# Optimization experiments

Measured on AMD Instinct MI355X. Metric: run time of the kernel, lower is better.

The kernel has to match this reference:

```python
import jax, jax.numpy as jnp
import numpy as np
import math

B, S, D, NH, HFF, E, K, C, L, V = 8, 256, 1024, 16, 2048, 8, 2, 10, 4, 32000
HD = D // NH
EPS = 1e-5


def _pos_encoding(max_len, d_model):
    pos = jnp.arange(max_len, dtype=jnp.float32)[:, None]
    div = jnp.exp(jnp.arange(0, d_model, 2, dtype=jnp.float32) * (-math.log(10000.0) / d_model))
    pe = jnp.zeros((max_len, d_model), dtype=jnp.float32)
    pe = pe.at[:, 0::2].set(jnp.sin(pos * div))
    pe = pe.at[:, 1::2].set(jnp.cos(pos * div))
    return pe[:, None, :]  # [max_len, 1, D], matching torch buffer layout


def _layernorm(x, g, b):
    mu = jnp.mean(x, axis=-1, keepdims=True)
    var = jnp.mean((x - mu) ** 2, axis=-1, keepdims=True)
    return (x - mu) * jax.lax.rsqrt(var + EPS) * g + b


def setup_inputs() -> dict:
    key = jax.random.key(0)
    ks = jax.random.split(key, 20)
    sc = lambda *shape: 0.02
    inp = {
        "src": jax.random.randint(ks[0], (B, S), 0, V, dtype=jnp.int32),
        "emb": jax.random.normal(ks[1], (V, D), jnp.float32) * 0.02,
        "in_proj_w": jax.random.normal(ks[2], (L, 3 * D, D), jnp.float32) * 0.02,
        "in_proj_b": jnp.zeros((L, 3 * D), jnp.float32),
        "out_w": jax.random.normal(ks[3], (L, D, D), jnp.float32) * 0.02,
        "out_b": jnp.zeros((L, D), jnp.float32),
        "ln1_g": jnp.ones((L, D), jnp.float32),
        "ln1_b": jnp.zeros((L, D), jnp.float32),
        "ln2_g": jnp.ones((L, D), jnp.float32),
        "ln2_b": jnp.zeros((L, D), jnp.float32),
        "gate_w": jax.random.normal(ks[4], (L, E, D), jnp.float32) * 0.02,
        "gate_b": jnp.zeros((L, E), jnp.float32),
        "w1": jax.random.normal(ks[5], (L, E, D, HFF), jnp.float32) * 0.02,
        "b1": jnp.zeros((L, E, HFF), jnp.float32),
        "w2": jax.random.normal(ks[6], (L, E, HFF, D), jnp.float32) * 0.02,
        "b2": jnp.zeros((L, E, D), jnp.float32),
        "cls_w": jax.random.normal(ks[7], (C, D), jnp.float32) * 0.02,
        "cls_b": jnp.zeros((C,), jnp.float32),
    }
    return inp


def _attention(x, ipw, ipb, ow, ob):
    # x: [B,S,D]
    qkv = x @ ipw.T + ipb  # [B,S,3D]
    q, k, v = jnp.split(qkv, 3, axis=-1)
    q = q.reshape(B, S, NH, HD)
    k = k.reshape(B, S, NH, HD)
    v = v.reshape(B, S, NH, HD)
    scores = jnp.einsum("bqhd,bkhd->bhqk", q, k) / math.sqrt(HD)
    attn = jax.nn.softmax(scores, axis=-1)
    o = jnp.einsum("bhqk,bkhd->bqhd", attn, v).reshape(B, S, D)
    return o @ ow.T + ob


def _moe(x, gw, gb, w1, b1, w2, b2):
    # x: [B,S,D]; gw: [E,D]; w1: [E,D,H]; w2: [E,H,D]
    t = x.reshape(B * S, D)
    logits = t @ gw.T + gb  # [T,E]
    topv, topi = jax.lax.top_k(logits, K)  # [T,K]
    weights = jax.nn.softmax(topv, axis=-1)  # [T,K]
    # dense expert compute (small E, compute-bound), combine via top-k gather
    h = jax.nn.relu(jnp.einsum("td,edh->teh", t, w1) + b1)  # [T,E,H]
    y = jnp.einsum("teh,ehd->ted", h, w2) + b2  # [T,E,D]
    sel = jnp.take_along_axis(y, topi[:, :, None], axis=1)  # [T,K,D]
    out = jnp.sum(sel * weights[:, :, None], axis=1)  # [T,D]
    return out.reshape(B, S, D), logits.reshape(B, S, E)


def reference(src, emb, in_proj_w, in_proj_b, out_w, out_b, ln1_g, ln1_b,
              ln2_g, ln2_b, gate_w, gate_b, w1, b1, w2, b2, cls_w, cls_b):
    x = emb[src] * math.sqrt(D)  # [B,S,D]
    pe = _pos_encoding(5000, D)  # [max_len,1,D]
    # faithful to original: pe indexed by batch dim (x.size(0)), broadcast over seq
    x = x + pe[:B]  # [B,1,D] -> broadcast [B,S,D]
    all_gates = []
    for l in range(in_proj_w.shape[0]):
        a = _attention(x, in_proj_w[l], in_proj_b[l], out_w[l], out_b[l])
        x = _layernorm(x + a, ln1_g[l], ln1_b[l])
        m, g = _moe(x, gate_w[l], gate_b[l], w1[l], b1[l], w2[l], b2[l])
        x = _layernorm(x + m, ln2_g[l], ln2_b[l])
        all_gates.append(g)
    pooled = jnp.mean(x, axis=1)  # [B,D]
    out = pooled @ cls_w.T + cls_b  # [B,C]
    return out, jnp.stack(all_gates)  # ([B,C], [L,B,S,E])
```

## Files before the change

kernel.cpp:

```cpp
#include <hip/hip_runtime.h>
#include <math.h>

#define TKN 2048
#define DIM 1024
#define NHEAD 16
#define HDIM 64
#define HFF 2048
#define NE 8
#define TOPK 2
#define NCLS 10
#define NLAYER 4
#define SEQ 256
#define BATCH 8

typedef __attribute__((ext_vector_type(8))) _Float16 f16x8;
typedef __attribute__((ext_vector_type(4))) float f32x4;
typedef __attribute__((ext_vector_type(8))) unsigned short u16x8;

__device__ __forceinline__ unsigned short f2h(float v) {
  _Float16 h = (_Float16)v;
  return __builtin_bit_cast(unsigned short, h);
}
__device__ __forceinline__ float h2f(unsigned short u) {
  return (float)__builtin_bit_cast(_Float16, u);
}
__device__ __forceinline__ void fsplit(float v, unsigned short& hi, unsigned short& lo) {
  _Float16 h = (_Float16)v;
  hi = __builtin_bit_cast(unsigned short, h);
  lo = f2h(v - (float)h);
}

__device__ __forceinline__ void gload_lds16(const void* g, void* l) {
  __builtin_amdgcn_global_load_lds((__attribute__((address_space(1))) void*)g,
                                   (__attribute__((address_space(3))) void*)l,
                                   16, 0, 0);
}

__global__ __launch_bounds__(256) void k_embed(const int* __restrict__ src,
                                               const float* __restrict__ emb,
                                               float* __restrict__ x,
                                               unsigned short* __restrict__ xhi,
                                               unsigned short* __restrict__ xlo) {
  const int t = blockIdx.x;
  const int tid = threadIdx.x;
  const int b = t / SEQ;
  const int tok = src[t];
  const float* erow = emb + (size_t)tok * DIM;
  const size_t base = (size_t)t * DIM;
  const float cexp = -9.210340371976184f / 1024.0f;
#pragma unroll
  for (int j = 0; j < 4; ++j) {
    int d = tid + 256 * j;
    int i2 = d & ~1;
    float ang = (float)b * expf((float)i2 * cexp);
    float pe = (d & 1) ? cosf(ang) : sinf(ang);
    float v = erow[d] * 32.0f + pe;
    x[base + d] = v;
    fsplit(v, xhi[base + d], xlo[base + d]);
  }
}

template <bool LO>
__global__ __launch_bounds__(256) void k_cvt_split(const float* __restrict__ in,
                                                   unsigned short* __restrict__ ohi,
                                                   unsigned short* __restrict__ olo) {
  int i = blockIdx.x * 256 + threadIdx.x;
  float4 v = ((const float4*)in)[i];
  ushort4 h, l;
  fsplit(v.x, h.x, l.x); fsplit(v.y, h.y, l.y);
  fsplit(v.z, h.z, l.z); fsplit(v.w, h.w, l.w);
  ((ushort4*)ohi)[i] = h;
  if (LO) ((ushort4*)olo)[i] = l;
}

template <bool LO>
__global__ __launch_bounds__(256) void k_cvt_t2(const float* __restrict__ in,
                                                unsigned short* __restrict__ ohi,
                                                unsigned short* __restrict__ olo,
                                                int R, int Cc) {
  __shared__ float ts[64][33];
  const int t = threadIdx.x;
  const int c0 = blockIdx.x * 32, r0 = blockIdx.y * 64;
  const float* ip = in + (size_t)blockIdx.z * R * Cc;
  const size_t obase = (size_t)blockIdx.z * R * Cc;
  const int cc = t & 31, rr0 = t >> 5;
#pragma unroll
  for (int j = 0; j < 8; ++j)
    ts[rr0 + 8 * j][cc] = ip[(size_t)(r0 + rr0 + 8 * j) * Cc + c0 + cc];
  __syncthreads();
  const int c = t >> 3, rch = (t & 7) * 8;
  u16x8 hv, lv;
#pragma unroll
  for (int i = 0; i < 8; ++i) {
    unsigned short hi, lo;
    fsplit(ts[rch + i][c], hi, lo);
    hv[i] = hi; lv[i] = lo;
  }
  size_t o = obase + (size_t)(c0 + c) * R + r0 + rch;
  *(u16x8*)(ohi + o) = hv;
  if (LO) *(u16x8*)(olo + o) = lv;
}

template <int MODE, bool RELU, int OUTK, bool SPLIT>
__global__ __launch_bounds__(256) void k_mfma_gemm(
    const unsigned short* __restrict__ Ahi, const unsigned short* __restrict__ Alo,
    const unsigned short* __restrict__ Bhi, const unsigned short* __restrict__ Blo,
    const float* __restrict__ bias, void* __restrict__ out0, void* __restrict__ out1,
    int M, int N, int K,
    const int* __restrict__ slot_token, const int* __restrict__ offg) {
  constexpr int NP = SPLIT ? 2 : 1;
  __shared__ unsigned short U[2][NP][128 * 64];
  const int tid = threadIdx.x;
  const int w = tid >> 6, lane = tid & 63;
  const int bm = blockIdx.y * 128, bn = blockIdx.x * 128;
  int r0 = 0, rows = M, e = 0;
  if (MODE != 0) {
    e = blockIdx.z;
    r0 = offg[e];
    rows = offg[e + 1] - r0;
    if (bm >= rows) return;
  }
  const size_t bwb = (size_t)e * K * N;
  const float* biasq = bias + (size_t)e * N;

  const int lrow8 = lane >> 3;
  const int s = (lane & 7) ^ lrow8;
  const int chunk = (s & 3) * 8;
  const unsigned short* sp0[4];
  const unsigned short* sp1[4];
#pragma unroll
  for (int i = 0; i < 4; ++i) {
    int rloc = w * 32 + i * 8 + lrow8;
    int growA;
    if (MODE == 0) {
      growA = bm + rloc;
    } else {
      int rr = bm + rloc;
      if (rr >= rows) rr = rows - 1;
      growA = (MODE == 1) ? slot_token[r0 + rr] : (r0 + rr);
    }
    size_t aoff = (size_t)growA * K + chunk;
    size_t boff = bwb + (size_t)(bn + rloc) * K + chunk;
    if constexpr (SPLIT) {
      sp0[i] = (s < 4 ? Ahi : Alo) + aoff;
      sp1[i] = (s < 4 ? Bhi : Blo) + boff;
    } else {
      sp0[i] = (s < 4) ? (Ahi + aoff) : (Bhi + boff);
      sp1[i] = nullptr;
    }
  }

  f32x4 acc[4][4] = {};
  const int wr = w >> 1, wc = w & 1;
  const int lr = lane & 15, lg = lane >> 4;
  const int sw = lr & 7;
  unsigned aoffs[4], boffs[4];
#pragma unroll
  for (int m = 0; m < 4; ++m)
    aoffs[m] = (unsigned)((wr * 64 + m * 16 + lr) * 64 + ((lg ^ sw) * 8));
#pragma unroll
  for (int n = 0; n < 4; ++n)
    boffs[n] = (unsigned)((wc * 64 + n * 16 + lr) * 64 + ((lg ^ sw) * 8));

#pragma unroll
  for (int i = 0; i < 4; ++i) {
    gload_lds16(sp0[i], &U[0][0][(w * 32 + i * 8) * 64]);
    sp0[i] += 32;
    if constexpr (SPLIT) {
      gload_lds16(sp1[i], &U[0][1][(w * 32 + i * 8) * 64]);
      sp1[i] += 32;
    }
  }
  asm volatile("s_waitcnt vmcnt(0)" ::: "memory");
  __builtin_amdgcn_s_barrier();

  const int NT = K / 32;
#pragma unroll 2
  for (int t = 0; t < NT; ++t) {
    const int cur = t & 1;
    if (t + 1 < NT) {
#pragma unroll
      for (int i = 0; i < 4; ++i) {
        gload_lds16(sp0[i], &U[cur ^ 1][0][(w * 32 + i * 8) * 64]);
        sp0[i] += 32;
        if constexpr (SPLIT) {
          gload_lds16(sp1[i], &U[cur ^ 1][1][(w * 32 + i * 8) * 64]);
          sp1[i] += 32;
        }
      }
    }
    f16x8 afh[4], bfh[4], afl[4], bfl[4];
    if constexpr (SPLIT) {
#pragma unroll
      for (int m = 0; m < 4; ++m) afh[m] = *(const f16x8*)&U[cur][0][aoffs[m]];
#pragma unroll
      for (int m = 0; m < 4; ++m) afl[m] = *(const f16x8*)&U[cur][0][aoffs[m] ^ 32];
#pragma unroll
      for (int n = 0; n < 4; ++n) bfh[n] = *(const f16x8*)&U[cur][1][boffs[n]];
#pragma unroll
      for (int n = 0; n < 4; ++n) bfl[n] = *(const f16x8*)&U[cur][1][boffs[n] ^ 32];
    } else {
#pragma unroll
      for (int m = 0; m < 4; ++m) afh[m] = *(const f16x8*)&U[cur][0][aoffs[m]];
#pragma unroll
      for (int n = 0; n < 4; ++n) bfh[n] = *(const f16x8*)&U[cur][0][boffs[n] ^ 32];
    }
#pragma unroll
    for (int m = 0; m < 4; ++m)
#pragma unroll
      for (int n = 0; n < 4; ++n) {
        acc[m][n] = __builtin_amdgcn_mfma_f32_16x16x32_f16(afh[m], bfh[n], acc[m][n], 0, 0, 0);
        if constexpr (SPLIT) {
          acc[m][n] = __builtin_amdgcn_mfma_f32_16x16x32_f16(afh[m], bfl[n], acc[m][n], 0, 0, 0);
          acc[m][n] = __builtin_amdgcn_mfma_f32_16x16x32_f16(afl[m], bfh[n], acc[m][n], 0, 0, 0);
        }
      }
    asm volatile("s_waitcnt vmcnt(0)" ::: "memory");
    __builtin_amdgcn_s_barrier();
  }

  float bv[4];
#pragma unroll
  for (int n = 0; n < 4; ++n) bv[n] = biasq[bn + wc * 64 + n * 16 + lr];

#pragma unroll
  for (int m = 0; m < 4; ++m) {
#pragma unroll
    for (int j = 0; j < 4; ++j) {
      int rowg = bm + wr * 64 + m * 16 + lg * 4 + j;
      if (MODE != 0 && rowg >= rows) continue;
      size_t crow = (size_t)((MODE == 0) ? rowg : (r0 + rowg)) * N;
#pragma unroll
      for (int n = 0; n < 4; ++n) {
        float v = acc[m][n][j] + bv[n];
        if (RELU) v = fmaxf(v, 0.f);
        size_t o = crow + bn + wc * 64 + n * 16 + lr;
        if (OUTK == 0) {
          ((float*)out0)[o] = v;
        } else if (OUTK == 1) {
          ((unsigned short*)out0)[o] = f2h(v);
        } else {
          unsigned short hi, lo;
          fsplit(v, hi, lo);
          ((unsigned short*)out0)[o] = hi;
          ((unsigned short*)out1)[o] = lo;
        }
      }
    }
  }
}

__global__ __launch_bounds__(256) void k_attn(const float* __restrict__ qkv,
                                              unsigned short* __restrict__ ohi,
                                              unsigned short* __restrict__ olo) {
  const int qt = blockIdx.x;
  const int hh = blockIdx.y;
  const int bb = blockIdx.z;
  const int tid = threadIdx.x;
  __shared__ float qs[16][64];
  __shared__ float ps[16][256];
  const int t0 = bb * SEQ + qt * 16;
  for (int i = tid; i < 16 * 64; i += 256) {
    int qi = i >> 6, d = i & 63;
    qs[qi][d] = qkv[(size_t)(t0 + qi) * (3 * DIM) + hh * 64 + d];
  }
  __syncthreads();
  float s[16];
#pragma unroll
  for (int qi = 0; qi < 16; ++qi) s[qi] = 0.f;
  const float* krow = qkv + (size_t)(bb * SEQ + tid) * (3 * DIM) + DIM + hh * 64;
#pragma unroll 4
  for (int c = 0; c < 16; ++c) {
    float4 kv = *(const float4*)(krow + c * 4);
#pragma unroll
    for (int qi = 0; qi < 16; ++qi) {
      s[qi] += kv.x * qs[qi][c * 4 + 0] + kv.y * qs[qi][c * 4 + 1] +
               kv.z * qs[qi][c * 4 + 2] + kv.w * qs[qi][c * 4 + 3];
    }
  }
#pragma unroll
  for (int qi = 0; qi < 16; ++qi) ps[qi][tid] = s[qi] * 0.125f;
  __syncthreads();
  const int wv = tid >> 6, lane = tid & 63;
  for (int rr = wv; rr < 16; rr += 4) {
    float v[4];
#pragma unroll
    for (int j = 0; j < 4; ++j) v[j] = ps[rr][lane + 64 * j];
    float m = fmaxf(fmaxf(v[0], v[1]), fmaxf(v[2], v[3]));
    for (int msk = 32; msk; msk >>= 1) m = fmaxf(m, __shfl_xor(m, msk));
    float e[4], sum = 0.f;
#pragma unroll
    for (int j = 0; j < 4; ++j) { e[j] = expf(v[j] - m); sum += e[j]; }
    for (int msk = 32; msk; msk >>= 1) sum += __shfl_xor(sum, msk);
    float inv = 1.0f / sum;
#pragma unroll
    for (int j = 0; j < 4; ++j) ps[rr][lane + 64 * j] = e[j] * inv;
  }
  __syncthreads();
  const int qi0 = tid >> 6, d = tid & 63;
  float acc[4] = {0.f, 0.f, 0.f, 0.f};
  const float* vbase = qkv + (size_t)(bb * SEQ) * (3 * DIM) + 2 * DIM + hh * 64 + d;
  for (int k = 0; k < 256; ++k) {
    float vv = vbase[(size_t)k * (3 * DIM)];
    acc[0] += ps[qi0][k] * vv;
    acc[1] += ps[qi0 + 4][k] * vv;
    acc[2] += ps[qi0 + 8][k] * vv;
    acc[3] += ps[qi0 + 12][k] * vv;
  }
#pragma unroll
  for (int j = 0; j < 4; ++j) {
    size_t o = (size_t)(t0 + qi0 + 4 * j) * DIM + hh * 64 + d;
    fsplit(acc[j], ohi[o], olo[o]);
  }
}

__device__ __forceinline__ float block_reduce_sum(float v, float* red) {
  const int tid = threadIdx.x;
  red[tid] = v;
  __syncthreads();
  for (int s = 128; s > 0; s >>= 1) {
    if (tid < s) red[tid] += red[tid + s];
    __syncthreads();
  }
  float r = red[0];
  __syncthreads();
  return r;
}

__global__ __launch_bounds__(256) void k_add_ln(const float* __restrict__ xin,
                                                const float* __restrict__ add,
                                                const float* __restrict__ g,
                                                const float* __restrict__ bt,
                                                float* __restrict__ xout,
                                                unsigned short* __restrict__ xhi,
                                                unsigned short* __restrict__ xlo) {
  __shared__ float red[256];
  const int t = blockIdx.x, tid = threadIdx.x;
  const size_t base = (size_t)t * DIM;
  float v[4];
  float s = 0.f;
#pragma unroll
  for (int j = 0; j < 4; ++j) {
    int d = tid + 256 * j;
    v[j] = xin[base + d] + add[base + d];
    s += v[j];
  }
  float mean = block_reduce_sum(s, red) * (1.0f / DIM);
  float s2 = 0.f;
#pragma unroll
  for (int j = 0; j < 4; ++j) { float dv = v[j] - mean; s2 += dv * dv; }
  float var = block_reduce_sum(s2, red) * (1.0f / DIM);
  float rs = rsqrtf(var + 1e-5f);
#pragma unroll
  for (int j = 0; j < 4; ++j) {
    int d = tid + 256 * j;
    float o = (v[j] - mean) * rs * g[d] + bt[d];
    xout[base + d] = o;
    fsplit(o, xhi[base + d], xlo[base + d]);
  }
}

__global__ __launch_bounds__(256) void k_gate(const float* __restrict__ x,
                                              const float* __restrict__ gw,
                                              const float* __restrict__ gb,
                                              float* __restrict__ gout,
                                              int* __restrict__ topi,
                                              float* __restrict__ topw) {
  __shared__ float xs[DIM];
  __shared__ float lgs[NE];
  const int t = blockIdx.x, tid = threadIdx.x;
#pragma unroll
  for (int j = 0; j < 4; ++j) xs[tid + 256 * j] = x[(size_t)t * DIM + tid + 256 * j];
  __syncthreads();
  const int eg = tid >> 5, l32 = tid & 31;
  const float* wrow = gw + (size_t)eg * DIM;
  float p = 0.f;
  for (int j = 0; j < 32; ++j) {
    int d = l32 + 32 * j;
    p += xs[d] * wrow[d];
  }
  for (int m = 16; m; m >>= 1) p += __shfl_xor(p, m);
  if (l32 == 0) lgs[eg] = p;
  __syncthreads();
  if (tid < NE) {
    float v = lgs[tid] + gb[tid];
    gout[(size_t)t * NE + tid] = v;
    lgs[tid] = v;
  }
  __syncthreads();
  if (tid == 0) {
    int i0 = 0; float v0 = lgs[0];
    for (int i = 1; i < NE; ++i) if (lgs[i] > v0) { v0 = lgs[i]; i0 = i; }
    int i1 = -1; float v1 = -1e30f;
    for (int i = 0; i < NE; ++i) { if (i == i0) continue; if (lgs[i] > v1) { v1 = lgs[i]; i1 = i; } }
    float e1 = expf(v1 - v0);
    float w0 = 1.0f / (1.0f + e1);
    topi[2 * t] = i0; topi[2 * t + 1] = i1;
    topw[2 * t] = w0; topw[2 * t + 1] = e1 * w0;
  }
}

__global__ __launch_bounds__(512) void k_route(const int* __restrict__ topi,
                                               int* __restrict__ offg,
                                               int* __restrict__ slot_token,
                                               int* __restrict__ slot_of) {
  __shared__ int cnt_s[NE];
  __shared__ int off_s[NE + 1];
  const int tid = threadIdx.x;
  const int w = tid >> 6, lane = tid & 63;
  int c = 0;
  for (int i = lane; i < TKN * TOPK; i += 64) c += (topi[i] == w) ? 1 : 0;
  for (int m = 32; m; m >>= 1) c += __shfl_xor(c, m);
  if (lane == 0) cnt_s[w] = c;
  __syncthreads();
  if (tid == 0) {
    off_s[0] = 0;
    for (int e2 = 0; e2 < NE; ++e2) off_s[e2 + 1] = off_s[e2] + cnt_s[e2];
    for (int e2 = 0; e2 <= NE; ++e2) offg[e2] = off_s[e2];
  }
  __syncthreads();
  int base = off_s[w];
  for (int i0 = 0; i0 < TKN * TOPK; i0 += 64) {
    int i = i0 + lane;
    bool mm = (topi[i] == w);
    unsigned long long mask = __ballot(mm ? 1 : 0);
    int rank = __popcll(mask & ((1ull << lane) - 1ull));
    if (mm) {
      int slot = base + rank;
      slot_token[slot] = i >> 1;
      slot_of[i] = slot;
    }
    base += __popcll(mask);
  }
}

__global__ __launch_bounds__(256) void k_moe_combine_ln(const float* __restrict__ xin,
                                                        const float* __restrict__ y,
                                                        const float* __restrict__ topw,
                                                        const int* __restrict__ slot_of,
                                                        const float* __restrict__ g,
                                                        const float* __restrict__ bt,
                                                        float* __restrict__ xout,
                                                        unsigned short* __restrict__ xhi,
                                                        unsigned short* __restrict__ xlo) {
  __shared__ float red[256];
  const int t = blockIdx.x, tid = threadIdx.x;
  const float w0 = topw[2 * t], w1v = topw[2 * t + 1];
  const int s0 = slot_of[2 * t], s1 = slot_of[2 * t + 1];
  const size_t base = (size_t)t * DIM;
  float v[4];
  float s = 0.f;
#pragma unroll
  for (int j = 0; j < 4; ++j) {
    int d = tid + 256 * j;
    v[j] = xin[base + d] + w0 * y[(size_t)s0 * DIM + d] + w1v * y[(size_t)s1 * DIM + d];
    s += v[j];
  }
  float mean = block_reduce_sum(s, red) * (1.0f / DIM);
  float s2 = 0.f;
#pragma unroll
  for (int j = 0; j < 4; ++j) { float dv = v[j] - mean; s2 += dv * dv; }
  float var = block_reduce_sum(s2, red) * (1.0f / DIM);
  float rs = rsqrtf(var + 1e-5f);
#pragma unroll
  for (int j = 0; j < 4; ++j) {
    int d = tid + 256 * j;
    float o = (v[j] - mean) * rs * g[d] + bt[d];
    xout[base + d] = o;
    fsplit(o, xhi[base + d], xlo[base + d]);
  }
}

__global__ __launch_bounds__(256) void k_pool_cls(const float* __restrict__ x,
                                                  const float* __restrict__ cw,
                                                  const float* __restrict__ cb,
                                                  float* __restrict__ out) {
  __shared__ float pooled[DIM];
  const int b = blockIdx.x, tid = threadIdx.x;
  float a[4] = {0.f, 0.f, 0.f, 0.f};
  for (int s = 0; s < SEQ; ++s) {
    const float* row = x + (size_t)(b * SEQ + s) * DIM;
#pragma unroll
    for (int j = 0; j < 4; ++j) a[j] += row[tid + 256 * j];
  }
#pragma unroll
  for (int j = 0; j < 4; ++j) pooled[tid + 256 * j] = a[j] * (1.0f / SEQ);
  __syncthreads();
  const int wv = tid >> 6, lane = tid & 63;
  for (int c = wv; c < NCLS; c += 4) {
    float p = 0.f;
    for (int d = lane; d < DIM; d += 64) p += pooled[d] * cw[(size_t)c * DIM + d];
    for (int m = 32; m; m >>= 1) p += __shfl_xor(p, m);
    if (lane == 0) out[b * NCLS + c] = p + cb[c];
  }
}

extern "C" void kernel_launch(void* const* d_in, const int* in_sizes, int n_in,
                              void* d_out, int out_size, void* d_ws, size_t ws_size,
                              hipStream_t stream) {
  const int*   src  = (const int*)  d_in[0];
  const float* emb  = (const float*)d_in[1];
  const float* ipw  = (const float*)d_in[2];
  const float* ipb  = (const float*)d_in[3];
  const float* ow   = (const float*)d_in[4];
  const float* ob   = (const float*)d_in[5];
  const float* ln1g = (const float*)d_in[6];
  const float* ln1b = (const float*)d_in[7];
  const float* ln2g = (const float*)d_in[8];
  const float* ln2b = (const float*)d_in[9];
  const float* gw   = (const float*)d_in[10];
  const float* gb   = (const float*)d_in[11];
  const float* w1   = (const float*)d_in[12];
  const float* b1   = (const float*)d_in[13];
  const float* w2   = (const float*)d_in[14];
  const float* b2   = (const float*)d_in[15];
  const float* cw   = (const float*)d_in[16];
  const float* cb   = (const float*)d_in[17];
  float* out = (float*)d_out;

  char* ws = (char*)d_ws;
  size_t off = 0;
  auto carve = [&](size_t bytes) -> void* {
    void* p = ws + off;
    off += (bytes + 255) & ~(size_t)255;
    return p;
  };
  float*          x     = (float*)carve((size_t)TKN * DIM * 4);
  unsigned short* xhi   = (unsigned short*)carve((size_t)TKN * DIM * 2);
  unsigned short* xlo   = (unsigned short*)carve((size_t)TKN * DIM * 2);
  char*           bufQ  = (char*)carve((size_t)2 * TKN * TOPK * HFF * 2);
  float*          qkv   = (float*)bufQ;
  unsigned short* h_hi  = (unsigned short*)bufQ;
  unsigned short* h_lo  = (unsigned short*)(bufQ + (size_t)TKN * TOPK * HFF * 2);
  unsigned short* at_hi = (unsigned short*)carve((size_t)TKN * DIM * 2);
  unsigned short* at_lo = (unsigned short*)carve((size_t)TKN * DIM * 2);
  char*           bufP  = (char*)carve((size_t)TKN * TOPK * DIM * 4);
  float*          proj  = (float*)bufP;
  float*          ybuf  = (float*)bufP;
  unsigned short* wq_hi = (unsigned short*)carve((size_t)3 * DIM * DIM * 2);
  unsigned short* wq_lo = (unsigned short*)carve((size_t)3 * DIM * DIM * 2);
  unsigned short* wo_hi = (unsigned short*)carve((size_t)DIM * DIM * 2);
  unsigned short* wo_lo = (unsigned short*)carve((size_t)DIM * DIM * 2);
  unsigned short* wt_hi = (unsigned short*)carve((size_t)NE * DIM * HFF * 2);
  unsigned short* wt_lo = (unsigned short*)carve((size_t)NE * DIM * HFF * 2);
  float* topw       = (float*)carve((size_t)TKN * TOPK * 4);
  int*   topi       = (int*)  carve((size_t)TKN * TOPK * 4);
  int*   slot_token = (int*)  carve((size_t)TKN * TOPK * 4);
  int*   slot_of    = (int*)  carve((size_t)TKN * TOPK * 4);
  int*   offg       = (int*)  carve(64);

  k_embed<<<TKN, 256, 0, stream>>>(src, emb, x, xhi, xlo);

  for (int l = 0; l < NLAYER; ++l) {
    const float* ipw_l = ipw + (size_t)l * 3 * DIM * DIM;
    const float* ow_l  = ow  + (size_t)l * DIM * DIM;
    const float* w1_l  = w1  + (size_t)l * NE * DIM * HFF;
    const float* w2_l  = w2  + (size_t)l * NE * HFF * DIM;
    const bool spd = (l < 3);
    const bool spm = (l < 2);

    if (spd) {
      k_cvt_split<true><<<(3 * DIM * DIM) / 1024, 256, 0, stream>>>(ipw_l, wq_hi, wq_lo);
      k_cvt_split<true><<<(DIM * DIM) / 1024, 256, 0, stream>>>(ow_l, wo_hi, wo_lo);
    } else {
      k_cvt_split<false><<<(3 * DIM * DIM) / 1024, 256, 0, stream>>>(ipw_l, wq_hi, wq_lo);
      k_cvt_split<false><<<(DIM * DIM) / 1024, 256, 0, stream>>>(ow_l, wo_hi, wo_lo);
    }
    if (spm)
      k_cvt_t2<true><<<dim3(HFF / 32, DIM / 64, NE), 256, 0, stream>>>(w1_l, wt_hi, wt_lo, DIM, HFF);
    else
      k_cvt_t2<false><<<dim3(HFF / 32, DIM / 64, NE), 256, 0, stream>>>(w1_l, wt_hi, wt_lo, DIM, HFF);

    if (spd)
      k_mfma_gemm<0, false, 0, true><<<dim3(3 * DIM / 128, TKN / 128), 256, 0, stream>>>(
          xhi, xlo, wq_hi, wq_lo, ipb + (size_t)l * 3 * DIM, qkv, nullptr, TKN, 3 * DIM, DIM, nullptr, nullptr);
    else
      k_mfma_gemm<0, false, 0, false><<<dim3(3 * DIM / 128, TKN / 128), 256, 0, stream>>>(
          xhi, xlo, wq_hi, wq_lo, ipb + (size_t)l * 3 * DIM, qkv, nullptr, TKN, 3 * DIM, DIM, nullptr, nullptr);

    k_attn<<<dim3(SEQ / 16, NHEAD, BATCH), 256, 0, stream>>>(qkv, at_hi, at_lo);

    if (spd)
      k_mfma_gemm<0, false, 0, true><<<dim3(DIM / 128, TKN / 128), 256, 0, stream>>>(
          at_hi, at_lo, wo_hi, wo_lo, ob + (size_t)l * DIM, proj, nullptr, TKN, DIM, DIM, nullptr, nullptr);
    else
      k_mfma_gemm<0, false, 0, false><<<dim3(DIM / 128, TKN / 128), 256, 0, stream>>>(
          at_hi, at_lo, wo_hi, wo_lo, ob + (size_t)l * DIM, proj, nullptr, TKN, DIM, DIM, nullptr, nullptr);

    k_add_ln<<<TKN, 256, 0, stream>>>(x, proj, ln1g + l * DIM, ln1b + l * DIM, x, xhi, xlo);

    k_gate<<<TKN, 256, 0, stream>>>(x, gw + (size_t)l * NE * DIM, gb + l * NE,
                                    out + NCLS * BATCH + (size_t)l * TKN * NE, topi, topw);
    k_route<<<1, 512, 0, stream>>>(topi, offg, slot_token, slot_of);

    if (spm)
      k_mfma_gemm<1, true, 2, true><<<dim3(HFF / 128, TKN * TOPK / 128, NE), 256, 0, stream>>>(
          xhi, xlo, wt_hi, wt_lo, b1 + (size_t)l * NE * HFF, h_hi, h_lo, 0, HFF, DIM, slot_token, offg);
    else
      k_mfma_gemm<1, true, 1, false><<<dim3(HFF / 128, TKN * TOPK / 128, NE), 256, 0, stream>>>(
          xhi, xlo, wt_hi, wt_lo, b1 + (size_t)l * NE * HFF, h_hi, nullptr, 0, HFF, DIM, slot_token, offg);

    if (spm)
      k_cvt_t2<true><<<dim3(DIM / 32, HFF / 64, NE), 256, 0, stream>>>(w2_l, wt_hi, wt_lo, HFF, DIM);
    else
      k_cvt_t2<false><<<dim3(DIM / 32, HFF / 64, NE), 256, 0, stream>>>(w2_l, wt_hi, wt_lo, HFF, DIM);

    if (spm)
      k_mfma_gemm<2, false, 0, true><<<dim3(DIM / 128, TKN * TOPK / 128, NE), 256, 0, stream>>>(
          h_hi, h_lo, wt_hi, wt_lo, b2 + (size_t)l * NE * DIM, ybuf, nullptr, 0, DIM, HFF, nullptr, offg);
    else
      k_mfma_gemm<2, false, 0, false><<<dim3(DIM / 128, TKN * TOPK / 128, NE), 256, 0, stream>>>(
          h_hi, h_lo, wt_hi, wt_lo, b2 + (size_t)l * NE * DIM, ybuf, nullptr, 0, DIM, HFF, nullptr, offg);

    k_moe_combine_ln<<<TKN, 256, 0, stream>>>(x, ybuf, topw, slot_of,
                                              ln2g + l * DIM, ln2b + l * DIM, x, xhi, xlo);
  }
  k_pool_cls<<<BATCH, 256, 0, stream>>>(x, cw, cb, out);
}
```

Baseline: 1.450 ms.

## Overlap next-tile loads with compute in GEMM and fuse gate into add-layernorm

The GEMM main loop now waits only for the current tile's loads (partial vmcnt) before its barrier, so the prefetch of the next K tile stays in flight during the MFMA work instead of being drained at the end of each iteration. Separately, the gating projection and top-2 selection are folded into the residual-add layernorm kernel, computing the logits from registers and dropping one launch plus a re-read of x. The partial waitcnt depends on counting exactly how many loads each thread issued, and the initial load wait was removed, so correctness relies on those counts matching.

```diff
diff --git a/kernel.cpp b/kernel.cpp
--- a/kernel.cpp
+++ b/kernel.cpp
@@ -171,8 +171,6 @@
       sp1[i] += 32;
     }
   }
-  asm volatile("s_waitcnt vmcnt(0)" ::: "memory");
-  __builtin_amdgcn_s_barrier();
 
   const int NT = K / 32;
 #pragma unroll 2
@@ -188,7 +186,15 @@
           sp1[i] += 32;
         }
       }
-    }
+      if constexpr (SPLIT)
+        asm volatile("s_waitcnt vmcnt(8)" ::: "memory");
+      else
+        asm volatile("s_waitcnt vmcnt(4)" ::: "memory");
+    } else {
+      asm volatile("s_waitcnt vmcnt(0)" ::: "memory");
+    }
+    __builtin_amdgcn_s_barrier();
+
     f16x8 afh[4], bfh[4], afl[4], bfl[4];
     if constexpr (SPLIT) {
 #pragma unroll
@@ -215,7 +221,6 @@
           acc[m][n] = __builtin_amdgcn_mfma_f32_16x16x32_f16(afl[m], bfh[n], acc[m][n], 0, 0, 0);
         }
       }
-    asm volatile("s_waitcnt vmcnt(0)" ::: "memory");
     __builtin_amdgcn_s_barrier();
   }
 
@@ -327,14 +332,21 @@
   return r;
 }
 
-__global__ __launch_bounds__(256) void k_add_ln(const float* __restrict__ xin,
-                                                const float* __restrict__ add,
-                                                const float* __restrict__ g,
-                                                const float* __restrict__ bt,
-                                                float* __restrict__ xout,
-                                                unsigned short* __restrict__ xhi,
-                                                unsigned short* __restrict__ xlo) {
+__global__ __launch_bounds__(256) void k_add_ln_gate(const float* __restrict__ xin,
+                                                     const float* __restrict__ add,
+                                                     const float* __restrict__ g,
+                                                     const float* __restrict__ bt,
+                                                     const float* __restrict__ gw,
+                                                     const float* __restrict__ gb,
+                                                     float* __restrict__ xout,
+                                                     unsigned short* __restrict__ xhi,
+                                                     unsigned short* __restrict__ xlo,
+                                                     float* __restrict__ gout,
+                                                     int* __restrict__ topi,
+                                                     float* __restrict__ topw) {
   __shared__ float red[256];
+  __shared__ float pw[4][NE];
+  __shared__ float lgs[NE];
   const int t = blockIdx.x, tid = threadIdx.x;
   const size_t base = (size_t)t * DIM;
   float v[4];
@@ -351,41 +363,33 @@
   for (int j = 0; j < 4; ++j) { float dv = v[j] - mean; s2 += dv * dv; }
   float var = block_reduce_sum(s2, red) * (1.0f / DIM);
   float rs = rsqrtf(var + 1e-5f);
+  float o[4];
 #pragma unroll
   for (int j = 0; j < 4; ++j) {
     int d = tid + 256 * j;
-    float o = (v[j] - mean) * rs * g[d] + bt[d];
-    xout[base + d] = o;
-    fsplit(o, xhi[base + d], xlo[base + d]);
-  }
-}
-
-__global__ __launch_bounds__(256) void k_gate(const float* __restrict__ x,
-                                              const float* __restrict__ gw,
-                                              const float* __restrict__ gb,
-                                              float* __restrict__ gout,
-                                              int* __restrict__ topi,
-                                              float* __restrict__ topw) {
-  __shared__ float xs[DIM];
-  __shared__ float lgs[NE];
-  const int t = blockIdx.x, tid = threadIdx.x;
-#pragma unroll
-  for (int j = 0; j < 4; ++j) xs[tid + 256 * j] = x[(size_t)t * DIM + tid + 256 * j];
-  __syncthreads();
-  const int eg = tid >> 5, l32 = tid & 31;
-  const float* wrow = gw + (size_t)eg * DIM;
-  float p = 0.f;
-  for (int j = 0; j < 32; ++j) {
-    int d = l32 + 32 * j;
-    p += xs[d] * wrow[d];
-  }
-  for (int m = 16; m; m >>= 1) p += __shfl_xor(p, m);
-  if (l32 == 0) lgs[eg] = p;
+    o[j] = (v[j] - mean) * rs * g[d] + bt[d];
+    xout[base + d] = o[j];
+    fsplit(o[j], xhi[base + d], xlo[base + d]);
+  }
+  const int wv = tid >> 6, lane = tid & 63;
+  float p[NE];
+#pragma unroll
+  for (int e = 0; e < NE; ++e) {
+    float pe = 0.f;
+#pragma unroll
+    for (int j = 0; j < 4; ++j) pe += o[j] * gw[(size_t)e * DIM + tid + 256 * j];
+    for (int m = 32; m; m >>= 1) pe += __shfl_xor(pe, m);
+    p[e] = pe;
+  }
+  if (lane == 0) {
+#pragma unroll
+    for (int e = 0; e < NE; ++e) pw[wv][e] = p[e];
+  }
   __syncthreads();
   if (tid < NE) {
-    float v = lgs[tid] + gb[tid];
-    gout[(size_t)t * NE + tid] = v;
-    lgs[tid] = v;
+    float l = pw[0][tid] + pw[1][tid] + pw[2][tid] + pw[3][tid] + gb[tid];
+    gout[(size_t)t * NE + tid] = l;
+    lgs[tid] = l;
   }
   __syncthreads();
   if (tid == 0) {
@@ -587,10 +591,10 @@
       k_mfma_gemm<0, false, 0, false><<<dim3(DIM / 128, TKN / 128), 256, 0, stream>>>(
           at_hi, at_lo, wo_hi, wo_lo, ob + (size_t)l * DIM, proj, nullptr, TKN, DIM, DIM, nullptr, nullptr);
 
-    k_add_ln<<<TKN, 256, 0, stream>>>(x, proj, ln1g + l * DIM, ln1b + l * DIM, x, xhi, xlo);
-
-    k_gate<<<TKN, 256, 0, stream>>>(x, gw + (size_t)l * NE * DIM, gb + l * NE,
-                                    out + NCLS * BATCH + (size_t)l * TKN * NE, topi, topw);
+    k_add_ln_gate<<<TKN, 256, 0, stream>>>(x, proj, ln1g + l * DIM, ln1b + l * DIM,
+                                           gw + (size_t)l * NE * DIM, gb + l * NE,
+                                           x, xhi, xlo,
+                                           out + NCLS * BATCH + (size_t)l * TKN * NE, topi, topw);
     k_route<<<1, 512, 0, stream>>>(topi, offg, slot_token, slot_of);
 
     if (spm)
```

Measured after the change: 1.455 ms. About the same (+0.3%).
